# Performance work log

Measured on AMD Instinct MI355X. Metric: run time of the kernel, lower is better.

## Reference

```python
import jax, jax.numpy as jnp
import numpy as np

B, C, H, W = 16, 256, 48, 160
BASELINE = 0.54
REL_ELEV = 1.65
H_MEAN = 1.535


def setup_inputs() -> dict:
    key = jax.random.key(0)
    k = jax.random.split(key, 5)
    features = jax.random.normal(k[0], (B, C, H, W), dtype=jnp.float32)
    # realistic KITTI-style P2 (full-resolution intrinsics; forward divides rows 0:2 by 16)
    base = np.zeros((3, 4), np.float32)
    base[0, 0] = 721.5; base[1, 1] = 721.5
    base[0, 2] = 609.5; base[1, 2] = 172.8
    base[2, 2] = 1.0;   base[1, 3] = 0.2
    P2 = jnp.asarray(base)[None] + 0.5 * jax.random.uniform(k[1], (B, 3, 4), dtype=jnp.float32)
    w_disp = 0.05 * jax.random.normal(k[2], (1, C, 3, 3), dtype=jnp.float32)  # disp_create conv3x3
    b_disp = jnp.zeros((1,), jnp.float32)
    w_ext = 0.05 * jax.random.normal(k[3], (C, C + 1), dtype=jnp.float32)     # extract conv1x1 (O,I)
    b_ext = jnp.zeros((C,), jnp.float32)
    alpha = 0.5 * jnp.ones((1,), jnp.float32)  # nn.Parameter (init 0.0; nonzero to exercise path)
    return {"features": features, "P2": P2, "w_disp": w_disp, "b_disp": b_disp,
            "w_ext": w_ext, "b_ext": b_ext, "alpha": alpha}


def _grid_sample_border(feat, gx, gy):
    """Bilinear grid_sample, padding_mode='border', align_corners=True.
    feat: (B,C1,H,W); gx, gy: (B,H,W) in [-1,1]."""
    Bs, C1, Hs, Ws = feat.shape
    ix = jnp.clip((gx + 1.0) * 0.5 * (Ws - 1), 0.0, Ws - 1)
    iy = jnp.clip((gy + 1.0) * 0.5 * (Hs - 1), 0.0, Hs - 1)
    ix0 = jnp.floor(ix); iy0 = jnp.floor(iy)
    ix1 = jnp.minimum(ix0 + 1.0, Ws - 1); iy1 = jnp.minimum(iy0 + 1.0, Hs - 1)
    wx = (ix - ix0).reshape(Bs, 1, -1)
    wy = (iy - iy0).reshape(Bs, 1, -1)
    flat = feat.reshape(Bs, C1, Hs * Ws)

    def gather(f, yq, xq):
        idx = (yq * Ws + xq).astype(jnp.int32).reshape(-1)
        return f[:, idx]  # (C1, H*W)

    g = jax.vmap(gather)
    v00 = g(flat, iy0, ix0); v01 = g(flat, iy0, ix1)
    v10 = g(flat, iy1, ix0); v11 = g(flat, iy1, ix1)
    out = (v00 * (1 - wx) * (1 - wy) + v01 * wx * (1 - wy)
           + v10 * (1 - wx) * wy + v11 * wx * wy)
    return out.reshape(Bs, C1, Hs, Ws)


def reference(features, P2, w_disp, b_disp, w_ext, b_ext, alpha):
    x = features
    Bs = x.shape[0]
    P2 = P2.at[:, 0:2].set(P2[:, 0:2] / 16.0)
    # disp_create: conv3x3 -> tanh, then detach-scaled
    d = jax.lax.conv_general_dilated(x, w_disp, (1, 1), 'SAME',
                                     dimension_numbers=('NCHW', 'OIHW', 'NCHW'))
    d = jnp.tanh(d + b_disp[None, :, None, None])
    disp = 0.1 * (0.05 * d + 0.95 * jax.lax.stop_gradient(d))  # (B,1,H,W)

    yy = jnp.arange(H, dtype=jnp.float32)[None, :, None]  # (1,H,1): row index
    fy = P2[:, 1:2, 1:2]; cy = P2[:, 1:2, 2:3]; Ty = P2[:, 1:2, 3:4]  # (B,1,1)
    disparity = jax.nn.relu(fy * BASELINE * (yy - cy)
                            / (jnp.abs(fy * REL_ELEV + Ty) + 1e-10))  # (B,H,1)
    disparity = jnp.broadcast_to(disparity, (Bs, H, W))

    x_base = jnp.broadcast_to(jnp.linspace(-1.0, 1.0, W, dtype=jnp.float32)[None, None, :], (Bs, H, W))
    y_base = jnp.linspace(-1.0, 1.0, H, dtype=jnp.float32)[None, :, None]  # (1,H,1)
    y_shifts_base = jax.nn.relu(H_MEAN * (yy - cy) / (2.0 * (REL_ELEV - 0.5 * H_MEAN))) / (H * 0.5)
    y_shifts = y_shifts_base + disp[:, 0]  # (B,H,W)
    gy = y_base + y_shifts

    feats = jnp.concatenate([disparity[:, None], x], axis=1)  # (B,C+1,H,W)
    samp = _grid_sample_border(feats, x_base, gy)
    out = jnp.einsum('oc,bchw->bohw', w_ext, samp) + b_ext[None, :, None, None]
    return jax.nn.relu(x + out * alpha[0])
```

## Files before the change

kernel.cpp:

```cpp
#include <hip/hip_runtime.h>
#include <stdint.h>

#define NB 16
#define NC 256
#define NH 48
#define NW 160
#define HW (NH*NW)
#define NP (NB*HW)

static __device__ __forceinline__ unsigned short f2bf(float f){
  union { float f; uint32_t u; } v; v.f = f;
  uint32_t u = v.u;
  uint32_t r = (u + 0x7FFFu + ((u >> 16) & 1u)) >> 16;
  return (unsigned short)r;
}
static __device__ __forceinline__ float bf2f(unsigned short h){
  union { float f; uint32_t u; } v; v.u = ((uint32_t)h) << 16; return v.f;
}

__global__ __launch_bounds__(256) void kw_conv(const float* __restrict__ w_ext,
                                               const float* __restrict__ w_disp,
                                               unsigned short* __restrict__ WbF,
                                               unsigned short* __restrict__ WtapF){
  int d = blockIdx.x * 256 + threadIdx.x;
  if (blockIdx.x < 256){
    int j  = d & 7;
    int lane = (d >> 3) & 63;
    int mi = (d >> 9) & 3;
    int w  = (d >> 11) & 3;
    int ks = d >> 13;
    int m = w * 64 + mi * 16 + (lane & 15);
    int k = ks * 32 + (lane >> 4) * 8 + j;
    WbF[d] = f2bf(w_ext[m * 257 + 1 + k]);
  } else {
    int d2 = d - 65536;
    int j  = d2 & 7;
    int lane = (d2 >> 3) & 63;
    int ks = d2 >> 9;
    int tap = lane & 15;
    int k = ks * 32 + (lane >> 4) * 8 + j;
    WtapF[d2] = (tap < 9) ? f2bf(w_disp[k * 9 + tap]) : (unsigned short)0;
  }
}

typedef __attribute__((ext_vector_type(8))) short bf16x8;
typedef __attribute__((ext_vector_type(4))) float f32x4;

__global__ __launch_bounds__(256, 3) void kb_gemm(
    const float* __restrict__ x,
    const unsigned short* __restrict__ Wb,
    const unsigned short* __restrict__ Wtap,
    unsigned short* __restrict__ U,
    float* __restrict__ T)
{
  __shared__ __align__(16) unsigned short smem[8 * 2048];
  int bx = blockIdx.x;
  int b  = bx / 120;
  int nt = bx - b * 120;
  int p0 = nt * 64;

  int tid  = threadIdx.x;
  int lane = tid & 63;
  int w    = tid >> 6;
  int l15 = lane & 15;
  int lq  = lane >> 4;

  int q  = tid & 31;
  int cg = tid >> 5;
  const float* xb_u = x + (size_t)b * NC * HW + p0;
  uint32_t voff0 = ((uint32_t)cg * 32u * (uint32_t)HW + 2u * (uint32_t)q) * 4u;

  float2 v[32];
#define GL(i) asm volatile("global_load_dwordx2 %0, %1, %2"                   \
    : "=v"(v[i])                                                              \
    : "v"(voff0 + (uint32_t)((i) * HW * 4)), "s"(xb_u) : "memory")
  GL(0); GL(1); GL(2); GL(3); GL(4); GL(5); GL(6); GL(7);
  GL(8); GL(9); GL(10); GL(11); GL(12); GL(13); GL(14); GL(15);
  GL(16); GL(17); GL(18); GL(19); GL(20); GL(21); GL(22); GL(23);
  GL(24); GL(25); GL(26); GL(27); GL(28); GL(29); GL(30); GL(31);
#undef GL

  bf16x8 afA[4], afB[4];
  bf16x8 atA, atB = {0,0,0,0,0,0,0,0};
  #pragma unroll
  for (int mi = 0; mi < 4; ++mi)
    afA[mi] = *(const bf16x8*)(Wb + ((w * 4 + mi) << 9) + lane * 8);
  atA = *(const bf16x8*)(Wtap + lane * 8);

  f32x4 zero = {0.f, 0.f, 0.f, 0.f};
  f32x4 acc[4][4];
  f32x4 acct[4];
  #pragma unroll
  for (int mi = 0; mi < 4; ++mi){
    acct[mi] = zero;
    #pragma unroll
    for (int ni = 0; ni < 4; ++ni) acc[mi][ni] = zero;
  }

  int n0 = 2 * q;
  unsigned short* sw0 = smem + cg * 2048 + (n0 >> 4) * 512;
  int n15a = n0 & 15;
#define CVT_GROUP(g)                                                          \
  { unsigned short ha[8], hb[8];                                              \
    _Pragma("unroll")                                                         \
    for (int j = 0; j < 8; ++j){                                              \
      ha[j] = f2bf(v[8 * (g) + j].x);                                         \
      hb[j] = f2bf(v[8 * (g) + j].y);                                         \
    }                                                                         \
    *(bf16x8*)(sw0 + (n15a     + (g) * 16) * 8) = *(bf16x8*)ha;               \
    *(bf16x8*)(sw0 + (n15a + 1 + (g) * 16) * 8) = *(bf16x8*)hb;               \
  }

  asm volatile("s_waitcnt vmcnt(24)" ::: "memory");
  __builtin_amdgcn_sched_barrier(0);
  CVT_GROUP(0)
  asm volatile("s_waitcnt vmcnt(16)" ::: "memory");
  __builtin_amdgcn_sched_barrier(0);
  CVT_GROUP(1)
  asm volatile("s_waitcnt vmcnt(8)" ::: "memory");
  __builtin_amdgcn_sched_barrier(0);
  CVT_GROUP(2)
  asm volatile("s_waitcnt vmcnt(5)" ::: "memory");
  __builtin_amdgcn_sched_barrier(0);
  CVT_GROUP(3)
#undef CVT_GROUP

  asm volatile("s_waitcnt lgkmcnt(0)" ::: "memory");
  __builtin_amdgcn_sched_barrier(0);
  __builtin_amdgcn_s_barrier();
  __builtin_amdgcn_sched_barrier(0);

#define KB_STEP(T_, AFC, AFN, ATC, ATN)                                       \
  {                                                                           \
    constexpr int t_ = (T_);                                                  \
    if (t_ + 1 < 8) {                                                         \
      _Pragma("unroll")                                                       \
      for (int mi = 0; mi < 4; ++mi)                                          \
        AFN[mi] = *(const bf16x8*)(Wb + (((t_ + 1) * 16 + w * 4 + mi) << 9)   \
                                   + lane * 8);                               \
      if (w == 0)                                                             \
        ATN = *(const bf16x8*)(Wtap + ((t_ + 1) << 9) + lane * 8);            \
    }                                                                         \
    bf16x8 bg[4];                                                             \
    _Pragma("unroll")                                                         \
    for (int ni = 0; ni < 4; ++ni)                                            \
      bg[ni] = *(const bf16x8*)(smem + t_ * 2048 + ni * 512 + lane * 8);      \
    _Pragma("unroll")                                                         \
    for (int mi = 0; mi < 4; ++mi)                                            \
      _Pragma("unroll")                                                       \
      for (int ni = 0; ni < 4; ++ni)                                          \
        acc[mi][ni] = __builtin_amdgcn_mfma_f32_16x16x32_bf16(AFC[mi], bg[ni],\
                                                      acc[mi][ni], 0, 0, 0);  \
    if (w == 0) {                                                             \
      _Pragma("unroll")                                                       \
      for (int ni = 0; ni < 4; ++ni)                                          \
        acct[ni] = __builtin_amdgcn_mfma_f32_16x16x32_bf16(ATC, bg[ni],       \
                                                       acct[ni], 0, 0, 0);    \
    }                                                                         \
  }

  KB_STEP(0, afA, afB, atA, atB)
  KB_STEP(1, afB, afA, atB, atA)
  KB_STEP(2, afA, afB, atA, atB)
  KB_STEP(3, afB, afA, atB, atA)
  KB_STEP(4, afA, afB, atA, atB)
  KB_STEP(5, afB, afA, atB, atA)
  KB_STEP(6, afA, afB, atA, atB)
  KB_STEP(7, afB, afA, atB, atA)
#undef KB_STEP

  #pragma unroll
  for (int mi = 0; mi < 4; ++mi){
    #pragma unroll
    for (int ni = 0; ni < 4; ++ni){
      int o = w * 64 + mi * 16 + lq * 4;
      int n = ni * 16 + l15;
      size_t base = ((size_t)(b * NC + o)) * HW + p0 + n;
      #pragma unroll
      for (int r = 0; r < 4; ++r)
        U[base + (size_t)r * HW] = f2bf(acc[mi][ni][r]);
    }
  }
  if (w == 0){
    #pragma unroll
    for (int ni = 0; ni < 4; ++ni){
      int n = ni * 16 + l15;
      #pragma unroll
      for (int r = 0; r < 4; ++r){
        int k = lq * 4 + r;
        if (k < 9)
          T[(size_t)k * NP + (size_t)b * HW + p0 + n] = acct[ni][r];
      }
    }
  }
}

__global__ __launch_bounds__(256) void kp_grid(
    const float* __restrict__ P2, const float* __restrict__ b_disp,
    const float* __restrict__ T, float4* __restrict__ pre)
{
  int p = blockIdx.x * 256 + threadIdx.x;
  int b  = p / HW;
  int hw = p - b * HW;
  int y  = hw / NW;
  int xx = hw - y * NW;

  float d = 0.f;
  #pragma unroll
  for (int ky = 0; ky < 3; ++ky){
    int yy2 = y + ky - 1;
    if (yy2 < 0 || yy2 >= NH) continue;
    #pragma unroll
    for (int kx = 0; kx < 3; ++kx){
      int xx2 = xx + kx - 1;
      if (xx2 < 0 || xx2 >= NW) continue;
      d += T[(size_t)(ky * 3 + kx) * NP + b * HW + yy2 * NW + xx2];
    }
  }
  float th = tanhf(d + b_disp[0]);

  float fy = P2[b * 12 + 5] * 0.0625f;
  float cy = P2[b * 12 + 6] * 0.0625f;
  float Ty = P2[b * 12 + 7] * 0.0625f;

  float ysb   = fmaxf(1.535f * ((float)y - cy) / 1.765f, 0.f) * (1.f / 24.f);
  float ybase = -1.f + (float)y * (2.f / 47.f);
  float gy = ybase + ysb + 0.1f * th;
  float iy = fminf(fmaxf((gy + 1.f) * 0.5f * 47.f, 0.f), 47.f);
  float fiy0 = floorf(iy);
  float wy = iy - fiy0;
  int iy0 = (int)fiy0;
  int iy1 = min(iy0 + 1, 47);

  float inv_den = 1.f / (fabsf(fy * 1.65f + Ty) + 1e-10f);
  float dr0 = fmaxf(fy * 0.54f * ((float)iy0 - cy) * inv_den, 0.f);
  float dr1 = fmaxf(fy * 0.54f * ((float)iy1 - cy) * inv_den, 0.f);
  float dlerp = (1.f - wy) * dr0 + wy * dr1;

  float4 pr;
  pr.x = wy; pr.y = dlerp;
  pr.z = __int_as_float(iy0 * NW + xx);
  pr.w = __int_as_float(iy1 * NW + xx);
  pre[p] = pr;
}

__global__ __launch_bounds__(256) void kc_epilogue(
    const float* __restrict__ x, const float* __restrict__ w_ext,
    const float* __restrict__ b_ext, const float* __restrict__ alpha,
    const unsigned short* __restrict__ U, const float4* __restrict__ pre,
    float* __restrict__ out)
{
  int bx = blockIdx.x;
  int ptile = bx >> 3;
  int cg    = bx & 7;
  int p = ptile * 256 + threadIdx.x;
  int b  = p / HW;
  int hw = p - b * HW;

  float4 pr = pre[p];
  float wy    = pr.x;
  float dlerp = pr.y;
  int off0 = __float_as_int(pr.z);
  int off1 = __float_as_int(pr.w);
  float w1 = 1.f - wy;
  float al = alpha[0];

  size_t base0 = (size_t)(b * NC) * HW;
  const unsigned short* Ub = U + base0;
  const float* xb = x + base0 + hw;
  float* ob = out + base0 + hw;

  int o0 = cg * 32;
  #pragma unroll 4
  for (int o = o0; o < o0 + 32; ++o){
    float u0 = bf2f(Ub[(size_t)o * HW + off0]);
    float u1 = bf2f(Ub[(size_t)o * HW + off1]);
    float val = w1 * u0 + wy * u1 + w_ext[o * 257] * dlerp + b_ext[o];
    float r = xb[(size_t)o * HW] + al * val;
    ob[(size_t)o * HW] = fmaxf(r, 0.f);
  }
}

extern "C" void kernel_launch(void* const* d_in, const int* in_sizes, int n_in,
                              void* d_out, int out_size, void* d_ws, size_t ws_size,
                              hipStream_t stream) {
  const float* features = (const float*)d_in[0];
  const float* P2       = (const float*)d_in[1];
  const float* w_disp   = (const float*)d_in[2];
  const float* b_disp   = (const float*)d_in[3];
  const float* w_ext    = (const float*)d_in[4];
  const float* b_ext    = (const float*)d_in[5];
  const float* alpha    = (const float*)d_in[6];
  float* out = (float*)d_out;

  char* ws = (char*)d_ws;
  const size_t U_bytes   = (size_t)NP * 256 * 2;
  const size_t T_bytes   = (size_t)9 * NP * 4;
  const size_t pre_bytes = (size_t)NP * 16;
  unsigned short* U    = (unsigned short*)ws;
  float*          T    = (float*)(ws + U_bytes);
  float4*         pre  = (float4*)(ws + U_bytes + T_bytes);
  unsigned short* Wb   = (unsigned short*)(ws + U_bytes + T_bytes + pre_bytes);
  unsigned short* Wtap = Wb + 256 * 256;

  hipLaunchKernelGGL(kw_conv,     dim3(272),  dim3(256), 0, stream, w_ext, w_disp, Wb, Wtap);
  hipLaunchKernelGGL(kb_gemm,     dim3(1920), dim3(256), 0, stream, features, Wb, Wtap, U, T);
  hipLaunchKernelGGL(kp_grid,     dim3(480),  dim3(256), 0, stream, P2, b_disp, T, pre);
  hipLaunchKernelGGL(kc_epilogue, dim3(3840), dim3(256), 0, stream,
                     features, w_ext, b_ext, alpha, U, pre, out);
}
```

Before: 319.0 us.

## Interleave U in groups of four channels for vectorized bf16 stores and gathers

Changes the intermediate U buffer layout from channel-major planes to groups of four consecutive output channels stored together per pixel. The GEMM writes each 4-element accumulator fragment as one 8-byte store, and the gather kernel loads all 32 channels with 16 vector loads issued up front instead of 64 scalar gathers inside the loop. The GEMM launch bound is also relaxed from 3 to 2 waves per SIMD, which gives it more registers but lower occupancy. The up-front loads also raise register pressure in the gather kernel.

```diff
diff --git a/kernel.cpp b/kernel.cpp
--- a/kernel.cpp
+++ b/kernel.cpp
@@ -44,9 +44,10 @@
 }
 
 typedef __attribute__((ext_vector_type(8))) short bf16x8;
+typedef __attribute__((ext_vector_type(4))) short bf16x4;
 typedef __attribute__((ext_vector_type(4))) float f32x4;
 
-__global__ __launch_bounds__(256, 3) void kb_gemm(
+__global__ __launch_bounds__(256, 2) void kb_gemm(
     const float* __restrict__ x,
     const unsigned short* __restrict__ Wb,
     const unsigned short* __restrict__ Wtap,
@@ -171,14 +172,14 @@
 
   #pragma unroll
   for (int mi = 0; mi < 4; ++mi){
+    int og = w * 16 + mi * 4 + lq;
     #pragma unroll
     for (int ni = 0; ni < 4; ++ni){
-      int o = w * 64 + mi * 16 + lq * 4;
       int n = ni * 16 + l15;
-      size_t base = ((size_t)(b * NC + o)) * HW + p0 + n;
+      unsigned short h[4];
       #pragma unroll
-      for (int r = 0; r < 4; ++r)
-        U[base + (size_t)r * HW] = f2bf(acc[mi][ni][r]);
+      for (int r = 0; r < 4; ++r) h[r] = f2bf(acc[mi][ni][r]);
+      *(bf16x4*)(U + (((size_t)b * 64 + og) * HW + p0 + n) * 4) = *(bf16x4*)h;
     }
   }
   if (w == 0){
@@ -265,19 +266,31 @@
   float w1 = 1.f - wy;
   float al = alpha[0];
 
+  int og0 = cg * 8;
+  const unsigned short* Ua = U + (((size_t)b * 64 + og0) * HW) * 4;
+  bf16x4 ua[8], ub[8];
+  #pragma unroll
+  for (int i = 0; i < 8; ++i){
+    ua[i] = *(const bf16x4*)(Ua + ((size_t)i * HW + off0) * 4);
+    ub[i] = *(const bf16x4*)(Ua + ((size_t)i * HW + off1) * 4);
+  }
+
   size_t base0 = (size_t)(b * NC) * HW;
-  const unsigned short* Ub = U + base0;
   const float* xb = x + base0 + hw;
   float* ob = out + base0 + hw;
 
   int o0 = cg * 32;
-  #pragma unroll 4
-  for (int o = o0; o < o0 + 32; ++o){
-    float u0 = bf2f(Ub[(size_t)o * HW + off0]);
-    float u1 = bf2f(Ub[(size_t)o * HW + off1]);
-    float val = w1 * u0 + wy * u1 + w_ext[o * 257] * dlerp + b_ext[o];
-    float r = xb[(size_t)o * HW] + al * val;
-    ob[(size_t)o * HW] = fmaxf(r, 0.f);
+  #pragma unroll
+  for (int i = 0; i < 8; ++i){
+    #pragma unroll
+    for (int r = 0; r < 4; ++r){
+      int o = o0 + i * 4 + r;
+      float u0 = bf2f((unsigned short)ua[i][r]);
+      float u1 = bf2f((unsigned short)ub[i][r]);
+      float val = w1 * u0 + wy * u1 + w_ext[o * 257] * dlerp + b_ext[o];
+      float rr = xb[(size_t)o * HW] + al * val;
+      ob[(size_t)o * HW] = fmaxf(rr, 0.f);
+    }
   }
 }
 
```

Measured after the change: 292.2 us. -8.4%, faster.
